# Optimization experiments

Hardware: AMD Instinct MI355X
Metric: run time of the kernel (lower is better)

Reference implementation:

```python
import jax, jax.numpy as jnp
import numpy as np

TOP_K = 8


def setup_inputs() -> dict:
    key = jax.random.key(0)
    k1, k2, k3 = jax.random.split(key, 3)
    N, D, SQRT_K = 8192, 2048, 64
    x = jax.random.normal(k1, (N, D), dtype=jnp.float32)
    W1 = jax.random.normal(k2, (SQRT_K, D), dtype=jnp.float32) * (1.0 / np.sqrt(D))
    W2 = jax.random.normal(k3, (SQRT_K, D), dtype=jnp.float32) * (1.0 / np.sqrt(D))
    return {"x": x, "W1": W1, "W2": W2}


def reference(x, W1, W2):
    # Two small projections: [N, d] @ [d, sqrt_K] -> [N, sqrt_K]
    s1 = jnp.einsum('nd,kd->nk', x, W1)
    s2 = jnp.einsum('nd,kd->nk', x, W2)
    # Outer-sum score matrix: expert (i, j) scores s1[i] + s2[j]; flatten -> [N, sqrt_K^2]
    scores = (s1[:, :, None] + s2[:, None, :]).reshape(x.shape[0], -1)
    topk_vals, topk_idx = jax.lax.top_k(scores, TOP_K)
    probs = jax.nn.softmax(topk_vals, axis=-1)
    return topk_idx, probs, scores
```

## Files before the change

kernel.cpp:

```cpp
#include <hip/hip_runtime.h>
#include <math.h>

#define NROWS 8192
#define DDIM  2048
#define NEXP  4096
#define TK    8
#define KSPLIT 4
#define KRANGE (DDIM / KSPLIT)
#define RB     32

typedef float  f4 __attribute__((ext_vector_type(4)));
typedef double d2 __attribute__((ext_vector_type(2)));

__global__ __launch_bounds__(256, 4) void pkr_gemm64(const float* __restrict__ x,
                                                     const float* __restrict__ w1,
                                                     const float* __restrict__ w2,
                                                     float* __restrict__ out) {
  __shared__ double xsd[32][34];
  __shared__ float  wsf[32][132];

  const int tid   = threadIdx.x;
  const int rb    = blockIdx.x >> 2;
  const int kp    = blockIdx.x & 3;
  const int rows0 = rb * RB;
  const int kbase = kp * KRANGE;

  const int rh = tid >> 5;
  const int ch = tid & 31;

  const int sxr = tid >> 3;
  const int sxk = (tid & 7) * 4;
  const float* xrow = x + (size_t)(rows0 + sxr) * DDIM + kbase + sxk;

  double acc[4][4] = {};

  for (int cch = 0; cch < KRANGE / 32; ++cch) {
    const int k0 = cch * 32;
    f4 xv = *(const f4*)(xrow + k0);
#pragma unroll
    for (int q = 0; q < 4; ++q) xsd[sxk + q][sxr] = (double)xv[q];
#pragma unroll
    for (int i = 0; i < 4; ++i) {
      const int idx = i * 256 + tid;
      const int c2  = idx >> 3;
      const int kk  = (idx & 7) * 4;
      const float* wr = (c2 < 64) ? (w1 + (size_t)c2 * DDIM)
                                  : (w2 + (size_t)(c2 - 64) * DDIM);
      f4 wv = *(const f4*)(wr + kbase + k0 + kk);
#pragma unroll
      for (int q = 0; q < 4; ++q) wsf[kk + q][c2] = wv[q];
    }
    __syncthreads();

#pragma unroll
    for (int k = 0; k < 32; ++k) {
      const d2 x01 = *(const d2*)&xsd[k][rh * 4];
      const d2 x23 = *(const d2*)&xsd[k][rh * 4 + 2];
      const f4 wq  = *(const f4*)&wsf[k][ch * 4];
      const double xd[4] = { x01[0], x01[1], x23[0], x23[1] };
      double wd[4];
#pragma unroll
      for (int b = 0; b < 4; ++b) wd[b] = (double)wq[b];
#pragma unroll
      for (int a = 0; a < 4; ++a)
#pragma unroll
        for (int b = 0; b < 4; ++b)
          acc[a][b] += xd[a] * wd[b];
    }
    __syncthreads();
  }

  double* P = (double*)(out + (size_t)2 * NROWS * TK);
#pragma unroll
  for (int a = 0; a < 4; ++a) {
    double* dst = P + (size_t)(rows0 + rh * 4 + a) * (NEXP / 2) + kp * 128 + ch * 4;
    d2 lo; lo[0] = acc[a][0]; lo[1] = acc[a][1];
    d2 hi; hi[0] = acc[a][2]; hi[1] = acc[a][3];
    *(d2*)dst       = lo;
    *(d2*)(dst + 2) = hi;
  }
}

__global__ __launch_bounds__(64) void pkr_finish(float* __restrict__ out) {
  const int row  = blockIdx.x;
  const int lane = threadIdx.x;

  const double* Pr = (const double*)(out + (size_t)2 * NROWS * TK) + (size_t)row * (NEXP / 2);
  double s1 = 0.0, s2 = 0.0;
#pragma unroll
  for (int p = 0; p < KSPLIT; ++p) {
    s1 += Pr[p * 128 + lane];
    s2 += Pr[p * 128 + 64 + lane];
  }

  __shared__ double sh1[64], sh2[64];
  sh1[lane] = s1;
  sh2[lane] = s2;
  __syncthreads();

  {
    float* srow = out + (size_t)2 * NROWS * TK + (size_t)row * NEXP;
    const int il = lane >> 4;
    const int jq = (lane & 15) * 4;
    const double sj0 = sh2[jq + 0], sj1 = sh2[jq + 1];
    const double sj2 = sh2[jq + 2], sj3 = sh2[jq + 3];
#pragma unroll
    for (int i0 = 0; i0 < 64; i0 += 4) {
      const double si = sh1[i0 + il];
      f4 v;
      v[0] = (float)(si + sj0);
      v[1] = (float)(si + sj1);
      v[2] = (float)(si + sj2);
      v[3] = (float)(si + sj3);
      *(f4*)(srow + (size_t)(i0 + il) * 64 + jq) = v;
    }
  }

  double av[8]; int ai[8];
  {
    double cur = s1;
#pragma unroll
    for (int t = 0; t < 8; ++t) {
      double bv = cur; int bi = lane;
#pragma unroll
      for (int off = 32; off; off >>= 1) {
        double ov = __shfl_xor(bv, off);
        int    oi = __shfl_xor(bi, off);
        if (ov > bv || (ov == bv && oi < bi)) { bv = ov; bi = oi; }
      }
      av[t] = bv; ai[t] = bi;
      if (lane == bi) cur = -INFINITY;
    }
  }
  double bv8[8]; int bi8[8];
  {
    double cur = s2;
#pragma unroll
    for (int t = 0; t < 8; ++t) {
      double bv = cur; int bi = lane;
#pragma unroll
      for (int off = 32; off; off >>= 1) {
        double ov = __shfl_xor(bv, off);
        int    oi = __shfl_xor(bi, off);
        if (ov > bv || (ov == bv && oi < bi)) { bv = ov; bi = oi; }
      }
      bv8[t] = bv; bi8[t] = bi;
      if (lane == bi) cur = -INFINITY;
    }
  }
  const double cval = av[lane >> 3] + bv8[lane & 7];
  const int    cidx = ai[lane >> 3] * 64 + bi8[lane & 7];
  double vvv[8]; int vidx[8];
  {
    double cur = cval;
#pragma unroll
    for (int t = 0; t < 8; ++t) {
      double bv = cur; int bi = cidx;
#pragma unroll
      for (int off = 32; off; off >>= 1) {
        double ov = __shfl_xor(bv, off);
        int    oi = __shfl_xor(bi, off);
        if (ov > bv || (ov == bv && oi < bi)) { bv = ov; bi = oi; }
      }
      vvv[t] = bv; vidx[t] = bi;
      if (cidx == bi) cur = -INFINITY;
    }
  }

  if (lane == 0) {
    float e[8], sum = 0.f;
#pragma unroll
    for (int t = 0; t < 8; ++t) { e[t] = expf((float)(vvv[t] - vvv[0])); sum += e[t]; }
    const float inv = 1.0f / sum;
#pragma unroll
    for (int t = 0; t < 8; ++t) {
      out[(size_t)row * TK + t]                       = (float)vidx[t];
      out[(size_t)NROWS * TK + (size_t)row * TK + t]  = e[t] * inv;
    }
  }
}

extern "C" void kernel_launch(void* const* d_in, const int* in_sizes, int n_in,
                              void* d_out, int out_size, void* d_ws, size_t ws_size,
                              hipStream_t stream) {
  const float* x  = (const float*)d_in[0];
  const float* w1 = (const float*)d_in[1];
  const float* w2 = (const float*)d_in[2];
  float* out = (float*)d_out;

  hipLaunchKernelGGL(pkr_gemm64, dim3((NROWS / RB) * KSPLIT), dim3(256), 0, stream,
                     x, w1, w2, out);
  hipLaunchKernelGGL(pkr_finish, dim3(NROWS), dim3(64), 0, stream, out);
}
```

Before: 298.5 us.

## Replace iterative top-k wave reductions with bitonic sorts and pack four rows per block

Drops the three 8-round argmax loops (8 butterfly reductions each) in the finish kernel and replaces them with full 64-lane bitonic sorts of s1, s2 and the 64 candidate sums. The softmax is now computed across lanes and written by 8 lanes instead of serially by lane 0. The finish kernel also handles four rows per 256-thread block instead of one row per 64-thread block, which cuts the block count. A bitonic sort uses 21 compare-exchange stages against 24 reduction steps, so shuffle work is similar, but it removes the serial tail work. Tie-breaking and ordering have to match the reference exactly.

```diff
diff --git a/kernel.cpp b/kernel.cpp
--- a/kernel.cpp
+++ b/kernel.cpp
@@ -81,9 +81,25 @@
   }
 }
 
-__global__ __launch_bounds__(64) void pkr_finish(float* __restrict__ out) {
-  const int row  = blockIdx.x;
-  const int lane = threadIdx.x;
+__device__ __forceinline__ void bitonic64(double& v, int& idx, int lane) {
+#pragma unroll
+  for (int k = 2; k <= 64; k <<= 1) {
+#pragma unroll
+    for (int j = k >> 1; j > 0; j >>= 1) {
+      const double ov = __shfl_xor(v, j);
+      const int    oi = __shfl_xor(idx, j);
+      const bool obetter = (ov > v) || (ov == v && oi < idx);
+      const bool lower   = (lane & j) == 0;
+      const bool up      = (lane & k) == 0;
+      if ((lower == up) ? obetter : !obetter) { v = ov; idx = oi; }
+    }
+  }
+}
+
+__global__ __launch_bounds__(256) void pkr_finish(float* __restrict__ out) {
+  const int lane = threadIdx.x & 63;
+  const int wv   = threadIdx.x >> 6;
+  const int row  = blockIdx.x * 4 + wv;
 
   const double* Pr = (const double*)(out + (size_t)2 * NROWS * TK) + (size_t)row * (NEXP / 2);
   double s1 = 0.0, s2 = 0.0;
@@ -93,20 +109,20 @@
     s2 += Pr[p * 128 + 64 + lane];
   }
 
-  __shared__ double sh1[64], sh2[64];
-  sh1[lane] = s1;
-  sh2[lane] = s2;
+  __shared__ double sh1[4][64], sh2[4][64];
+  sh1[wv][lane] = s1;
+  sh2[wv][lane] = s2;
   __syncthreads();
 
   {
     float* srow = out + (size_t)2 * NROWS * TK + (size_t)row * NEXP;
     const int il = lane >> 4;
     const int jq = (lane & 15) * 4;
-    const double sj0 = sh2[jq + 0], sj1 = sh2[jq + 1];
-    const double sj2 = sh2[jq + 2], sj3 = sh2[jq + 3];
+    const double sj0 = sh2[wv][jq + 0], sj1 = sh2[wv][jq + 1];
+    const double sj2 = sh2[wv][jq + 2], sj3 = sh2[wv][jq + 3];
 #pragma unroll
     for (int i0 = 0; i0 < 64; i0 += 4) {
-      const double si = sh1[i0 + il];
+      const double si = sh1[wv][i0 + il];
       f4 v;
       v[0] = (float)(si + sj0);
       v[1] = (float)(si + sj1);
@@ -116,67 +132,27 @@
     }
   }
 
-  double av[8]; int ai[8];
-  {
-    double cur = s1;
+  double v1 = s1; int i1 = lane;
+  bitonic64(v1, i1, lane);
+  double v2 = s2; int i2 = lane;
+  bitonic64(v2, i2, lane);
+
+  const double ca = __shfl(v1, lane >> 3);
+  const int    ia = __shfl(i1, lane >> 3);
+  const double cb = __shfl(v2, lane & 7);
+  const int    ib = __shfl(i2, lane & 7);
+  double cv = ca + cb;
+  int    ci = ia * 64 + ib;
+  bitonic64(cv, ci, lane);
+
+  const double vmax = __shfl(cv, 0);
+  float e = expf((float)(cv - vmax));
+  float sum = e;
 #pragma unroll
-    for (int t = 0; t < 8; ++t) {
-      double bv = cur; int bi = lane;
-#pragma unroll
-      for (int off = 32; off; off >>= 1) {
-        double ov = __shfl_xor(bv, off);
-        int    oi = __shfl_xor(bi, off);
-        if (ov > bv || (ov == bv && oi < bi)) { bv = ov; bi = oi; }
-      }
-      av[t] = bv; ai[t] = bi;
-      if (lane == bi) cur = -INFINITY;
-    }
-  }
-  double bv8[8]; int bi8[8];
-  {
-    double cur = s2;
-#pragma unroll
-    for (int t = 0; t < 8; ++t) {
-      double bv = cur; int bi = lane;
-#pragma unroll
-      for (int off = 32; off; off >>= 1) {
-        double ov = __shfl_xor(bv, off);
-        int    oi = __shfl_xor(bi, off);
-        if (ov > bv || (ov == bv && oi < bi)) { bv = ov; bi = oi; }
-      }
-      bv8[t] = bv; bi8[t] = bi;
-      if (lane == bi) cur = -INFINITY;
-    }
-  }
-  const double cval = av[lane >> 3] + bv8[lane & 7];
-  const int    cidx = ai[lane >> 3] * 64 + bi8[lane & 7];
-  double vvv[8]; int vidx[8];
-  {
-    double cur = cval;
-#pragma unroll
-    for (int t = 0; t < 8; ++t) {
-      double bv = cur; int bi = cidx;
-#pragma unroll
-      for (int off = 32; off; off >>= 1) {
-        double ov = __shfl_xor(bv, off);
-        int    oi = __shfl_xor(bi, off);
-        if (ov > bv || (ov == bv && oi < bi)) { bv = ov; bi = oi; }
-      }
-      vvv[t] = bv; vidx[t] = bi;
-      if (cidx == bi) cur = -INFINITY;
-    }
-  }
-
-  if (lane == 0) {
-    float e[8], sum = 0.f;
-#pragma unroll
-    for (int t = 0; t < 8; ++t) { e[t] = expf((float)(vvv[t] - vvv[0])); sum += e[t]; }
-    const float inv = 1.0f / sum;
-#pragma unroll
-    for (int t = 0; t < 8; ++t) {
-      out[(size_t)row * TK + t]                       = (float)vidx[t];
-      out[(size_t)NROWS * TK + (size_t)row * TK + t]  = e[t] * inv;
-    }
+  for (int off = 1; off < 8; off <<= 1) sum += __shfl_xor(sum, off);
+  if (lane < 8) {
+    out[(size_t)row * TK + lane]                      = (float)ci;
+    out[(size_t)NROWS * TK + (size_t)row * TK + lane] = e / sum;
   }
 }
 
@@ -190,5 +166,5 @@
 
   hipLaunchKernelGGL(pkr_gemm64, dim3((NROWS / RB) * KSPLIT), dim3(256), 0, stream,
                      x, w1, w2, out);
-  hipLaunchKernelGGL(pkr_finish, dim3(NROWS), dim3(64), 0, stream, out);
+  hipLaunchKernelGGL(pkr_finish, dim3(NROWS / 4), dim3(256), 0, stream, out);
 }
```

Measured after the change: 280.6 us. -6.0%, faster.
